# Kernel optimization log

Measured on AMD Instinct MI355X. Metric: run time of the kernel, lower is better.

The kernel has to match this reference:

```python
import jax, jax.numpy as jnp
import numpy as np

B, S, D, H = 2, 2048, 1024, 16
DK = D // H


def setup_inputs() -> dict:
    key = jax.random.key(0)
    ks = jax.random.split(key, 11)
    scale = 1.0 / np.sqrt(D)
    inp = {
        "k": jax.random.normal(ks[0], (B, S, D), jnp.float32),
        "q": jax.random.normal(ks[1], (B, S, D), jnp.float32),
        "v": jax.random.normal(ks[2], (B, S, D), jnp.float32),
        "w_q": jax.random.normal(ks[3], (D, D), jnp.float32) * scale,
        "b_q": jax.random.normal(ks[4], (D,), jnp.float32) * 0.01,
        "w_k": jax.random.normal(ks[5], (D, D), jnp.float32) * scale,
        "b_k": jax.random.normal(ks[6], (D,), jnp.float32) * 0.01,
        "w_v": jax.random.normal(ks[7], (D, D), jnp.float32) * scale,
        "b_v": jax.random.normal(ks[8], (D,), jnp.float32) * 0.01,
        "w_o": jax.random.normal(ks[9], (D, D), jnp.float32) * scale,
        "b_o": jax.random.normal(ks[10], (D,), jnp.float32) * 0.01,
        # causal mask; positions with mask==0 get -1e9 (masked_fill semantics)
        "mask": jnp.tril(jnp.ones((1, 1, S, S), jnp.int32)),
    }
    return inp


def reference(k, q, v, w_q, b_q, w_k, b_k, w_v, b_v, w_o, b_o, mask):
    MINUS_INF = -1000000000.0

    def proj(x, w, b):
        # nn.Linear: x @ w.T + b, then split heads -> [B, H, S, DK]
        y = x @ w.T + b
        return y.reshape(B, S, H, DK).transpose(0, 2, 1, 3)

    Q = proj(q, w_q, b_q)
    K = proj(k, w_k, b_k)
    V = proj(v, w_v, b_v)

    # [B, H, Sq, Sk] scores
    scores = jnp.einsum("bhqd,bhkd->bhqk", Q, K) / jnp.sqrt(jnp.float32(DK))
    scores = jnp.where(mask == 0, MINUS_INF, scores)
    attn = jax.nn.softmax(scores, axis=-1)

    out = jnp.einsum("bhqk,bhkd->bhqd", attn, V)  # [B, H, S, DK]
    out = out.transpose(0, 2, 1, 3).reshape(B, S, D)  # concat heads
    return out @ w_o.T + b_o
```

## Files before the change

### kernel.cpp

```cpp
#include <hip/hip_runtime.h>

typedef __bf16 bf16;
typedef __bf16 v8bf __attribute__((ext_vector_type(8)));
typedef __bf16 v4bf __attribute__((ext_vector_type(4)));
typedef float  v4f  __attribute__((ext_vector_type(4)));

#define MFMA16(a,b,c) __builtin_amdgcn_mfma_f32_16x16x32_bf16((a),(b),(c),0,0,0)

static constexpr int Sq = 2048;
static constexpr size_t NI = 4194304;
static constexpr size_t NW = 1048576;

__device__ __forceinline__ void gld_lds16(const void* g, void* l) {
  __builtin_amdgcn_global_load_lds(
      (__attribute__((address_space(1))) unsigned int*)g,
      (__attribute__((address_space(3))) unsigned int*)l,
      16, 0, 0);
}

__global__ __launch_bounds__(256) void convert_kernel(
    const float* __restrict__ q, const float* __restrict__ k, const float* __restrict__ v,
    const float* __restrict__ wq, const float* __restrict__ wk,
    const float* __restrict__ wv, const float* __restrict__ wo,
    bf16* __restrict__ dst)
{
  const int NI4 = 1048576;
  const int NW4 = 262144;
  int idx = blockIdx.x * 256 + threadIdx.x;
  const float* src; size_t dstoff; int local;
  if (idx < 3 * NI4) {
    int a = idx >> 20; local = idx & (NI4 - 1);
    src = (a == 0) ? q : ((a == 1) ? k : v);
    dstoff = (size_t)a * NI;
  } else {
    int t = idx - 3 * NI4;
    int a = t >> 18; local = t & (NW4 - 1);
    src = (a == 0) ? wq : ((a == 1) ? wk : ((a == 2) ? wv : wo));
    dstoff = 3 * NI + (size_t)a * NW;
  }
  float4 f = ((const float4*)src)[local];
  v4bf hv = { (bf16)f.x, (bf16)f.y, (bf16)f.z, (bf16)f.w };
  *(v4bf*)(dst + dstoff + (size_t)local * 4) = hv;
}

__device__ __forceinline__ void gemm_bt_body(
    const bf16* __restrict__ A, const bf16* __restrict__ Bw,
    const float* __restrict__ bias, bf16* __restrict__ outh,
    float* __restrict__ outf, int bm, int bn, int mode)
{
  __shared__ alignas(16) bf16 As[128 * 32];
  __shared__ alignas(16) bf16 Bs[128 * 32];
  const int tid = threadIdx.x;
  const int wave = tid >> 6, lane = tid & 63;
  const int quad = lane >> 4, l15 = lane & 15;
  const int wm = (wave >> 1) * 64, wn = (wave & 1) * 64;
  const int lrow = lane >> 2, lcol = (lane & 3) * 8;

  v4f acc[4][4];
#pragma unroll
  for (int i = 0; i < 4; i++)
#pragma unroll
    for (int j = 0; j < 4; j++) { v4f z = {0.f, 0.f, 0.f, 0.f}; acc[i][j] = z; }

  const bf16* gA = A  + (size_t)(bm + wave * 32 + lrow) * 1024 + lcol;
  const bf16* gB = Bw + (size_t)(bn + wave * 32 + lrow) * 1024 + lcol;
  bf16* lA0 = &As[(wave * 32) * 32];
  bf16* lA1 = &As[(wave * 32 + 16) * 32];
  bf16* lB0 = &Bs[(wave * 32) * 32];
  bf16* lB1 = &Bs[(wave * 32 + 16) * 32];

  for (int k0 = 0; k0 < 1024; k0 += 32) {
    gld_lds16(gA + k0, lA0);
    gld_lds16(gA + 16 * 1024 + k0, lA1);
    gld_lds16(gB + k0, lB0);
    gld_lds16(gB + 16 * 1024 + k0, lB1);
    __syncthreads();
    v8bf af[4], bfr[4];
#pragma unroll
    for (int i = 0; i < 4; i++)
      af[i] = *(const v8bf*)&As[(wm + i * 16 + l15) * 32 + quad * 8];
#pragma unroll
    for (int j = 0; j < 4; j++)
      bfr[j] = *(const v8bf*)&Bs[(wn + j * 16 + l15) * 32 + quad * 8];
#pragma unroll
    for (int i = 0; i < 4; i++)
#pragma unroll
      for (int j = 0; j < 4; j++)
        acc[i][j] = MFMA16(af[i], bfr[j], acc[i][j]);
    __syncthreads();
  }

#pragma unroll
  for (int i = 0; i < 4; i++) {
    const int m0 = bm + wm + i * 16 + quad * 4;
#pragma unroll
    for (int j = 0; j < 4; j++) {
      const int n = bn + wn + j * 16 + l15;
      const float bv = bias[n];
      if (mode == 1) {
#pragma unroll
        for (int r = 0; r < 4; r++)
          outf[(size_t)(m0 + r) * 1024 + n] = acc[i][j][r] + bv;
      } else if (mode == 2) {
        int b_ = m0 >> 11, s_ = m0 & 2047;
        int h_ = n >> 6,  dk = n & 63;
        v4bf pk;
#pragma unroll
        for (int r = 0; r < 4; r++) pk[r] = (bf16)(acc[i][j][r] + bv);
        *(v4bf*)&outh[((size_t)((b_ * 16 + h_) * 64 + dk)) * 2048 + s_] = pk;
      } else {
        const float sc = (mode == 3) ? 0.125f : 1.0f;
        int h_ = n >> 6,  dk = n & 63;
#pragma unroll
        for (int r = 0; r < 4; r++) {
          int m = m0 + r;
          int b_ = m >> 11, s_ = m & 2047;
          outh[(((size_t)(b_ * 16 + h_) * 2048 + s_) << 6) + dk] =
              (bf16)((acc[i][j][r] + bv) * sc);
        }
      }
    }
  }
}

__global__ __launch_bounds__(256, 2) void gemm_proj_kernel(
    const bf16* qb, const bf16* kb, const bf16* vb,
    const bf16* wqb, const bf16* wkb, const bf16* wvb,
    const float* bq, const float* bk, const float* bv,
    bf16* Qh, bf16* Kh, bf16* VhT)
{
  const bf16* A; const bf16* W; const float* bias; bf16* out; int mode;
  if (blockIdx.z == 0)      { A = qb; W = wqb; bias = bq; out = Qh;  mode = 3; }
  else if (blockIdx.z == 1) { A = kb; W = wkb; bias = bk; out = Kh;  mode = 0; }
  else                      { A = vb; W = wvb; bias = bv; out = VhT; mode = 2; }
  gemm_bt_body(A, W, bias, out, nullptr, blockIdx.y * 128, blockIdx.x * 128, mode);
}

__global__ __launch_bounds__(256, 2) void gemm_final_kernel(
    const bf16* Ob, const bf16* wob, const float* bo, float* out)
{
  gemm_bt_body(Ob, wob, bo, nullptr, out, blockIdx.y * 128, blockIdx.x * 128, 1);
}

__global__ __launch_bounds__(128, 2) void attn_kernel(
    const bf16* __restrict__ Qh, const bf16* __restrict__ Kh,
    const bf16* __restrict__ VhT, bf16* __restrict__ Ob)
{
  __shared__ alignas(16) bf16 Ps[2][32 * 72];
  const int tid = threadIdx.x;
  const int wave = tid >> 6, lane = tid & 63;
  const int quad = lane >> 4, l15 = lane & 15;
  const int bh = blockIdx.x, gy = blockIdx.y;
  const int b = bh >> 4, h = bh & 15;
  const int r8 = gy & 7, q8 = gy >> 3;
  const int u = 8 * q8 + ((q8 & 1) ? (7 - r8) : r8);
  const int qt = 2 * u + wave;
  const int L = u;
  const bf16* Qb = Qh + (size_t)bh * Sq * 64;
  const bf16* Kb = Kh + (size_t)bh * Sq * 64;
  const bf16* Vb = VhT + (size_t)bh * 64 * Sq;
  bf16* Pw = &Ps[wave][0];
  const int r0 = qt * 32;

  v8bf aq[2][2];
#pragma unroll
  for (int s = 0; s < 2; s++)
#pragma unroll
    for (int ks = 0; ks < 2; ks++)
      aq[s][ks] = *(const v8bf*)&Qb[(size_t)(r0 + s * 16 + l15) * 64 + ks * 32 + quad * 8];

  float lsum[2][4];
  v4f o[2][4];
#pragma unroll
  for (int s = 0; s < 2; s++)
#pragma unroll
    for (int r = 0; r < 4; r++) lsum[s][r] = 0.f;
#pragma unroll
  for (int s = 0; s < 2; s++)
#pragma unroll
    for (int j = 0; j < 4; j++) { v4f z = {0.f, 0.f, 0.f, 0.f}; o[s][j] = z; }

  auto loadK = [&](int kb, v8bf (&BK)[4][2]) {
#pragma unroll
    for (int n = 0; n < 4; n++) {
      BK[n][0] = *(const v8bf*)&Kb[(size_t)(kb + n * 16 + l15) * 64 + quad * 8];
      BK[n][1] = *(const v8bf*)&Kb[(size_t)(kb + n * 16 + l15) * 64 + 32 + quad * 8];
    }
  };
  auto loadV = [&](int kb, v8bf (&BV)[4][2]) {
#pragma unroll
    for (int n = 0; n < 4; n++) {
      BV[n][0] = *(const v8bf*)&Vb[(size_t)(n * 16 + l15) * 2048 + kb + quad * 8];
      BV[n][1] = *(const v8bf*)&Vb[(size_t)(n * 16 + l15) * 2048 + kb + 32 + quad * 8];
    }
  };
  auto compute = [&](const v8bf (&BK)[4][2], const v8bf (&BV)[4][2], int kc) {
    const int kbase = kc * 64;
    const bool diag = (kc == L);
#pragma unroll
    for (int s = 0; s < 2; s++) {
      v4f cn[4];
#pragma unroll
      for (int n = 0; n < 4; n++) {
        v4f z = {0.f, 0.f, 0.f, 0.f};
        cn[n] = MFMA16(aq[s][0], BK[n][0], z);
        cn[n] = MFMA16(aq[s][1], BK[n][1], cn[n]);
      }
      const int rbase = r0 + s * 16 + quad * 4;
#pragma unroll
      for (int n = 0; n < 4; n++) {
        const int colg = kbase + n * 16 + l15;
#pragma unroll
        for (int r = 0; r < 4; r++) {
          float e = __expf(cn[n][r]);
          if (diag && colg > rbase + r) e = 0.f;
          lsum[s][r] += e;
          Pw[(s * 16 + quad * 4 + r) * 72 + n * 16 + l15] = (bf16)e;
        }
      }
    }
#pragma unroll
    for (int s = 0; s < 2; s++) {
      v8bf ap0 = *(const v8bf*)&Pw[(s * 16 + l15) * 72 + quad * 8];
      v8bf ap1 = *(const v8bf*)&Pw[(s * 16 + l15) * 72 + 32 + quad * 8];
#pragma unroll
      for (int j = 0; j < 4; j++) {
        o[s][j] = MFMA16(ap0, BV[j][0], o[s][j]);
        o[s][j] = MFMA16(ap1, BV[j][1], o[s][j]);
      }
    }
  };

  v8bf bk0[4][2], bk1[4][2], bvv[4][2];
  loadK(0, bk0);
  int kc = 0;
  while (true) {
    loadV(kc * 64, bvv);
    if (kc < L) loadK((kc + 1) * 64, bk1);
    compute(bk0, bvv, kc);
    if (++kc > L) break;
    loadV(kc * 64, bvv);
    if (kc < L) loadK((kc + 1) * 64, bk0);
    compute(bk1, bvv, kc);
    if (++kc > L) break;
  }

#pragma unroll
  for (int s = 0; s < 2; s++)
#pragma unroll
    for (int r = 0; r < 4; r++) {
#pragma unroll
      for (int off = 1; off < 16; off <<= 1)
        lsum[s][r] += __shfl_xor(lsum[s][r], off, 64);
    }
#pragma unroll
  for (int s = 0; s < 2; s++)
#pragma unroll
    for (int r = 0; r < 4; r++) {
      const float inv = 1.0f / lsum[s][r];
      const int sg = r0 + s * 16 + quad * 4 + r;
#pragma unroll
      for (int j = 0; j < 4; j++)
        Ob[((size_t)(b * Sq + sg)) * 1024 + h * 64 + j * 16 + l15] =
            (bf16)(o[s][j][r] * inv);
    }
}

extern "C" void kernel_launch(void* const* d_in, const int* in_sizes, int n_in,
                              void* d_out, int out_size, void* d_ws, size_t ws_size,
                              hipStream_t stream) {
  (void)in_sizes; (void)n_in; (void)out_size; (void)ws_size;
  const float* kin = (const float*)d_in[0];
  const float* qin = (const float*)d_in[1];
  const float* vin = (const float*)d_in[2];
  const float* wq  = (const float*)d_in[3];
  const float* bq  = (const float*)d_in[4];
  const float* wk  = (const float*)d_in[5];
  const float* bk  = (const float*)d_in[6];
  const float* wv  = (const float*)d_in[7];
  const float* bv  = (const float*)d_in[8];
  const float* wo  = (const float*)d_in[9];
  const float* bo  = (const float*)d_in[10];

  bf16* ws = (bf16*)d_ws;
  bf16* qb  = ws;
  bf16* kb  = ws + NI;
  bf16* vb  = ws + 2 * NI;
  bf16* wqb = ws + 3 * NI;
  bf16* wkb = wqb + NW;
  bf16* wvb = wqb + 2 * NW;
  bf16* wob = wqb + 3 * NW;
  bf16* Qh  = ws + 3 * NI + 4 * NW;
  bf16* Kh  = Qh + NI;
  bf16* VhT = Qh + 2 * NI;
  bf16* Ob  = Qh + 3 * NI;

  convert_kernel<<<16384, 256, 0, stream>>>(qin, kin, vin, wq, wk, wv, wo, ws);
  gemm_proj_kernel<<<dim3(8, 32, 3), 256, 0, stream>>>(
      qb, kb, vb, wqb, wkb, wvb, bq, bk, bv, Qh, Kh, VhT);
  attn_kernel<<<dim3(32, 32), 128, 0, stream>>>(Qh, Kh, VhT, Ob);
  gemm_final_kernel<<<dim3(8, 32), 256, 0, stream>>>(Ob, wob, bo, (float*)d_out);
}
```

Baseline: 267.1 us.

## Split long causal attention rows across two blocks with combine kernel, use exp2

Query tiles in the second half of the sequence have their key range split into two blocks (first 16 key chunks and the rest). Each block writes unnormalised fp32 partial outputs and row sums, and a new combine kernel adds them and normalises. This balances work across blocks in causal attention. The Q scale now folds in log2(e) so exp2f can replace __expf, and s_setprio is raised around the MFMA groups. The cost is an extra kernel launch plus the fp32 partial writes and reads.

```diff
diff --git a/kernel.cpp b/kernel.cpp
--- a/kernel.cpp
+++ b/kernel.cpp
@@ -109,7 +109,7 @@
         for (int r = 0; r < 4; r++) pk[r] = (bf16)(acc[i][j][r] + bv);
         *(v4bf*)&outh[((size_t)((b_ * 16 + h_) * 64 + dk)) * 2048 + s_] = pk;
       } else {
-        const float sc = (mode == 3) ? 0.125f : 1.0f;
+        const float sc = (mode == 3) ? 0.18033688011112042f : 1.0f;
         int h_ = n >> 6,  dk = n & 63;
 #pragma unroll
         for (int r = 0; r < 4; r++) {
@@ -144,18 +144,33 @@
 
 __global__ __launch_bounds__(128, 2) void attn_kernel(
     const bf16* __restrict__ Qh, const bf16* __restrict__ Kh,
-    const bf16* __restrict__ VhT, bf16* __restrict__ Ob)
+    const bf16* __restrict__ VhT, bf16* __restrict__ Ob,
+    float* __restrict__ po, float* __restrict__ plsum)
 {
   __shared__ alignas(16) bf16 Ps[2][32 * 72];
   const int tid = threadIdx.x;
   const int wave = tid >> 6, lane = tid & 63;
   const int quad = lane >> 4, l15 = lane & 15;
-  const int bh = blockIdx.x, gy = blockIdx.y;
+  const int bh = blockIdx.x, slot = blockIdx.y;
   const int b = bh >> 4, h = bh & 15;
-  const int r8 = gy & 7, q8 = gy >> 3;
-  const int u = 8 * q8 + ((q8 & 1) ? (7 - r8) : r8);
-  const int qt = 2 * u + wave;
-  const int L = u;
+
+  int t, kc0, part;
+  if (slot < 16) {
+    t = (slot < 8) ? slot : 23 - slot;
+    kc0 = 0; part = -1;
+  } else if (slot < 32) {
+    int c = slot - 16;
+    t = 16 + ((c < 8) ? c : 23 - c);
+    kc0 = 0; part = 0;
+  } else {
+    int c = slot - 32;
+    t = 16 + ((c < 8) ? c : 23 - c);
+    kc0 = 16; part = 1;
+  }
+  const int qt  = 2 * t + wave;
+  const int kcL = (part == 0) ? 15 : t;
+  const bool hasDiag = (part != 0);
+
   const bf16* Qb = Qh + (size_t)bh * Sq * 64;
   const bf16* Kb = Kh + (size_t)bh * Sq * 64;
   const bf16* Vb = VhT + (size_t)bh * 64 * Sq;
@@ -196,23 +211,25 @@
   };
   auto compute = [&](const v8bf (&BK)[4][2], const v8bf (&BV)[4][2], int kc) {
     const int kbase = kc * 64;
-    const bool diag = (kc == L);
+    const bool diag = hasDiag && (kc == kcL);
 #pragma unroll
     for (int s = 0; s < 2; s++) {
       v4f cn[4];
+      __builtin_amdgcn_s_setprio(1);
 #pragma unroll
       for (int n = 0; n < 4; n++) {
         v4f z = {0.f, 0.f, 0.f, 0.f};
         cn[n] = MFMA16(aq[s][0], BK[n][0], z);
         cn[n] = MFMA16(aq[s][1], BK[n][1], cn[n]);
       }
+      __builtin_amdgcn_s_setprio(0);
       const int rbase = r0 + s * 16 + quad * 4;
 #pragma unroll
       for (int n = 0; n < 4; n++) {
         const int colg = kbase + n * 16 + l15;
 #pragma unroll
         for (int r = 0; r < 4; r++) {
-          float e = __expf(cn[n][r]);
+          float e = exp2f(cn[n][r]);
           if (diag && colg > rbase + r) e = 0.f;
           lsum[s][r] += e;
           Pw[(s * 16 + quad * 4 + r) * 72 + n * 16 + l15] = (bf16)e;
@@ -223,26 +240,28 @@
     for (int s = 0; s < 2; s++) {
       v8bf ap0 = *(const v8bf*)&Pw[(s * 16 + l15) * 72 + quad * 8];
       v8bf ap1 = *(const v8bf*)&Pw[(s * 16 + l15) * 72 + 32 + quad * 8];
+      __builtin_amdgcn_s_setprio(1);
 #pragma unroll
       for (int j = 0; j < 4; j++) {
         o[s][j] = MFMA16(ap0, BV[j][0], o[s][j]);
         o[s][j] = MFMA16(ap1, BV[j][1], o[s][j]);
       }
+      __builtin_amdgcn_s_setprio(0);
     }
   };
 
   v8bf bk0[4][2], bk1[4][2], bvv[4][2];
-  loadK(0, bk0);
-  int kc = 0;
+  loadK(kc0 * 64, bk0);
+  int kc = kc0;
   while (true) {
     loadV(kc * 64, bvv);
-    if (kc < L) loadK((kc + 1) * 64, bk1);
+    if (kc < kcL) loadK((kc + 1) * 64, bk1);
     compute(bk0, bvv, kc);
-    if (++kc > L) break;
+    if (++kc > kcL) break;
     loadV(kc * 64, bvv);
-    if (kc < L) loadK((kc + 1) * 64, bk0);
+    if (kc < kcL) loadK((kc + 1) * 64, bk0);
     compute(bk1, bvv, kc);
-    if (++kc > L) break;
+    if (++kc > kcL) break;
   }
 
 #pragma unroll
@@ -253,17 +272,59 @@
       for (int off = 1; off < 16; off <<= 1)
         lsum[s][r] += __shfl_xor(lsum[s][r], off, 64);
     }
-#pragma unroll
-  for (int s = 0; s < 2; s++)
-#pragma unroll
-    for (int r = 0; r < 4; r++) {
-      const float inv = 1.0f / lsum[s][r];
-      const int sg = r0 + s * 16 + quad * 4 + r;
+
+  if (part < 0) {
+#pragma unroll
+    for (int s = 0; s < 2; s++)
+#pragma unroll
+      for (int r = 0; r < 4; r++) {
+        const float inv = 1.0f / lsum[s][r];
+        const int sg = r0 + s * 16 + quad * 4 + r;
+#pragma unroll
+        for (int j = 0; j < 4; j++)
+          Ob[((size_t)(b * Sq + sg)) * 1024 + h * 64 + j * 16 + l15] =
+              (bf16)(o[s][j][r] * inv);
+      }
+  } else {
+    const size_t pidx = ((size_t)(bh * 32 + (qt - 32)) * 2 + part);
+    float* pob = po + pidx * 2048;
+#pragma unroll
+    for (int s = 0; s < 2; s++)
 #pragma unroll
       for (int j = 0; j < 4; j++)
-        Ob[((size_t)(b * Sq + sg)) * 1024 + h * 64 + j * 16 + l15] =
-            (bf16)(o[s][j][r] * inv);
-    }
+#pragma unroll
+        for (int r = 0; r < 4; r++)
+          pob[(s * 16 + quad * 4 + r) * 64 + j * 16 + l15] = o[s][j][r];
+    if (l15 == 0) {
+#pragma unroll
+      for (int s = 0; s < 2; s++)
+#pragma unroll
+        for (int r = 0; r < 4; r++)
+          plsum[pidx * 32 + s * 16 + quad * 4 + r] = lsum[s][r];
+    }
+  }
+}
+
+__global__ __launch_bounds__(256) void attn_combine_kernel(
+    const float* __restrict__ po, const float* __restrict__ plsum,
+    bf16* __restrict__ Ob)
+{
+  const int bh = blockIdx.x, ti = blockIdx.y;
+  const int b = bh >> 4, h = bh & 15;
+  const int tid = threadIdx.x;
+  const int col = tid & 63, rg = tid >> 6;
+  const size_t pidx = (size_t)(bh * 32 + ti) * 2;
+  const float* p0 = po + pidx * 2048;
+  const float* p1 = p0 + 2048;
+  const float* l0 = plsum + pidx * 32;
+#pragma unroll
+  for (int rr = 0; rr < 8; rr++) {
+    const int row = rg * 8 + rr;
+    const float inv = 1.0f / (l0[row] + l0[32 + row]);
+    const float v = p0[row * 64 + col] + p1[row * 64 + col];
+    const int sg = (32 + ti) * 32 + row;
+    Ob[((size_t)(b * 2048 + sg)) * 1024 + h * 64 + col] = (bf16)(v * inv);
+  }
 }
 
 extern "C" void kernel_launch(void* const* d_in, const int* in_sizes, int n_in,
@@ -294,10 +355,13 @@
   bf16* Kh  = Qh + NI;
   bf16* VhT = Qh + 2 * NI;
   bf16* Ob  = Qh + 3 * NI;
+  float* po    = (float*)(Ob + NI);
+  float* plsum = po + (size_t)32 * 32 * 2 * 2048;
 
   convert_kernel<<<16384, 256, 0, stream>>>(qin, kin, vin, wq, wk, wv, wo, ws);
   gemm_proj_kernel<<<dim3(8, 32, 3), 256, 0, stream>>>(
       qb, kb, vb, wqb, wkb, wvb, bq, bk, bv, Qh, Kh, VhT);
-  attn_kernel<<<dim3(32, 32), 128, 0, stream>>>(Qh, Kh, VhT, Ob);
+  attn_kernel<<<dim3(32, 48), 128, 0, stream>>>(Qh, Kh, VhT, Ob, po, plsum);
+  attn_combine_kernel<<<dim3(32, 32), 256, 0, stream>>>(po, plsum, Ob);
   gemm_final_kernel<<<dim3(8, 32), 256, 0, stream>>>(Ob, wob, bo, (float*)d_out);
 }
```

Result: slower. 277.3 us (+3.8%).

## Software-pipeline attention so QK softmax of next tile overlaps PV of current

Applied to the files above, without the earlier changes.

Splits the attention inner step into a QK+exp phase and a PV phase, with a double-buffered shared P tile and double-buffered V registers, so the next tile's QK/exp runs before the current tile's PV MFMAs. The goal is to hide MFMA and LDS latency behind each other. It also folds log2(e) into the Q scale and switches __expf to exp2f, dropping a multiply per element. The cost is higher register and LDS use, which could lower occupancy.

```diff
diff --git a/kernel.cpp b/kernel.cpp
--- a/kernel.cpp
+++ b/kernel.cpp
@@ -109,7 +109,7 @@
         for (int r = 0; r < 4; r++) pk[r] = (bf16)(acc[i][j][r] + bv);
         *(v4bf*)&outh[((size_t)((b_ * 16 + h_) * 64 + dk)) * 2048 + s_] = pk;
       } else {
-        const float sc = (mode == 3) ? 0.125f : 1.0f;
+        const float sc = (mode == 3) ? 0.18033688011112042f : 1.0f;
         int h_ = n >> 6,  dk = n & 63;
 #pragma unroll
         for (int r = 0; r < 4; r++) {
@@ -146,7 +146,7 @@
     const bf16* __restrict__ Qh, const bf16* __restrict__ Kh,
     const bf16* __restrict__ VhT, bf16* __restrict__ Ob)
 {
-  __shared__ alignas(16) bf16 Ps[2][32 * 72];
+  __shared__ alignas(16) bf16 Ps[2][2][32 * 72];
   const int tid = threadIdx.x;
   const int wave = tid >> 6, lane = tid & 63;
   const int quad = lane >> 4, l15 = lane & 15;
@@ -159,7 +159,6 @@
   const bf16* Qb = Qh + (size_t)bh * Sq * 64;
   const bf16* Kb = Kh + (size_t)bh * Sq * 64;
   const bf16* Vb = VhT + (size_t)bh * 64 * Sq;
-  bf16* Pw = &Ps[wave][0];
   const int r0 = qt * 32;
 
   v8bf aq[2][2];
@@ -194,7 +193,8 @@
       BV[n][1] = *(const v8bf*)&Vb[(size_t)(n * 16 + l15) * 2048 + kb + 32 + quad * 8];
     }
   };
-  auto compute = [&](const v8bf (&BK)[4][2], const v8bf (&BV)[4][2], int kc) {
+  auto qk_soft = [&](const v8bf (&BK)[4][2], int kc, int ph) {
+    bf16* Pw = &Ps[wave][ph][0];
     const int kbase = kc * 64;
     const bool diag = (kc == L);
 #pragma unroll
@@ -212,13 +212,16 @@
         const int colg = kbase + n * 16 + l15;
 #pragma unroll
         for (int r = 0; r < 4; r++) {
-          float e = __expf(cn[n][r]);
+          float e = exp2f(cn[n][r]);
           if (diag && colg > rbase + r) e = 0.f;
           lsum[s][r] += e;
           Pw[(s * 16 + quad * 4 + r) * 72 + n * 16 + l15] = (bf16)e;
         }
       }
     }
+  };
+  auto pv = [&](const v8bf (&BV)[4][2], int ph) {
+    bf16* Pw = &Ps[wave][ph][0];
 #pragma unroll
     for (int s = 0; s < 2; s++) {
       v8bf ap0 = *(const v8bf*)&Pw[(s * 16 + l15) * 72 + quad * 8];
@@ -231,19 +234,26 @@
     }
   };
 
-  v8bf bk0[4][2], bk1[4][2], bvv[4][2];
-  loadK(0, bk0);
-  int kc = 0;
-  while (true) {
-    loadV(kc * 64, bvv);
-    if (kc < L) loadK((kc + 1) * 64, bk1);
-    compute(bk0, bvv, kc);
-    if (++kc > L) break;
-    loadV(kc * 64, bvv);
-    if (kc < L) loadK((kc + 1) * 64, bk0);
-    compute(bk1, bvv, kc);
-    if (++kc > L) break;
+  v8bf k0[4][2], k1[4][2], v0[4][2], v1[4][2];
+  loadK(0, k0);
+  loadV(0, v0);
+  loadK(((L >= 1) ? 1 : 0) * 64, k1);
+  qk_soft(k0, 0, 0);
+
+  int c = 0;
+  while (c < L) {
+    if (c + 2 <= L) loadK((c + 2) * 64, k0);
+    qk_soft(k1, c + 1, 1);
+    loadV((c + 1) * 64, v1);
+    pv(v0, 0);
+    if (++c >= L) break;
+    if (c + 2 <= L) loadK((c + 2) * 64, k1);
+    qk_soft(k0, c + 1, 0);
+    loadV((c + 1) * 64, v0);
+    pv(v1, 1);
+    ++c;
   }
+  if (L & 1) pv(v1, 1); else pv(v0, 0);
 
 #pragma unroll
   for (int s = 0; s < 2; s++)
```

Result: slower. 347.9 us (+30.2%).
